# Kernel optimization log

Hardware: AMD Instinct MI355X
Metric: run time of the kernel (lower is better)

The kernel has to match this reference:

```python
import jax, jax.numpy as jnp
import numpy as np

D_MODEL, N, L_MAX, BATCH = 512, 64, 2048, 8


def _hippo_pq_lambda(n):
    # HiPPO-LegS matrix -> NPLR decomposition (numpy, done once at setup)
    i = np.arange(n)
    A = np.sqrt(2 * i + 1)[:, None] * np.sqrt(2 * i + 1)[None, :]
    A = np.tril(A, -1) + np.diag(i + 1.0)
    p0 = 0.5 * np.sqrt(2 * np.arange(1, n + 1) - 1.0)
    q0 = 2.0 * p0
    S = -A + p0[:, None] * q0[None, :]
    lam, V = np.linalg.eig(S)
    Vc = V.conj().T
    p = Vc @ p0.astype(np.complex128)
    q = Vc @ q0.astype(np.complex128)
    return lam, p, q


def _c2r(x):
    return np.stack([x.real, x.imag], axis=-1).astype(np.float32)


def setup_inputs() -> dict:
    key = jax.random.key(0)
    ks = jax.random.split(key, 6)
    lam, p, q = _hippo_pq_lambda(N)
    log_step_scale = float(np.log(0.1) - np.log(0.001))
    xavier_std = (2.0 / (D_MODEL + N)) ** 0.5
    return {
        "u": jax.random.normal(ks[0], (BATCH, L_MAX, D_MODEL), jnp.float32),
        "lam": jnp.asarray(_c2r(lam)),            # (N, 2) complex-as-real
        "p": jnp.asarray(_c2r(p)),                # (N, 2)
        "q": jnp.asarray(_c2r(q)),                # (N, 2)
        "B": jax.random.normal(ks[1], (D_MODEL, N, 2), jnp.float32) * xavier_std,
        "Ct": jax.random.normal(ks[2], (D_MODEL, N, 2), jnp.float32) * xavier_std,
        "D": jnp.ones((D_MODEL,), jnp.float32),
        "log_step": jax.random.uniform(ks[3], (D_MODEL,), jnp.float32) * log_step_scale + float(np.log(0.001)),
        "W": jax.random.normal(ks[4], (D_MODEL, D_MODEL), jnp.float32) / (D_MODEL ** 0.5),
        "b": jnp.zeros((D_MODEL,), jnp.float32),
        "gamma": jnp.ones((D_MODEL,), jnp.float32),
        "beta": jnp.zeros((D_MODEL,), jnp.float32),
    }


def _cplx(x):
    return x[..., 0] + 1j * x[..., 1]


def _s4_kernel(lam, p, q, B, Ct, step, l_max):
    # Generating function of the DPLR SSM kernel evaluated at roots of unity,
    # then inverse FFT -> length-l_max convolution kernel K, shape (d_model, l_max).
    omega = jnp.exp(2j * jnp.pi * jnp.arange(l_max) / l_max)  # (L,)
    a0, a1 = jnp.conj(Ct), jnp.conj(q)   # (d,n), (n,)
    b0, b1 = B, p                        # (d,n), (n,)
    v = jnp.stack([
        a0 * b0,
        a0 * b1[None, :],
        a1[None, :] * b0,
        jnp.broadcast_to((a1 * b1)[None, :], B.shape),
    ])  # (4, d, n)
    f = (2.0 / step)[:, None] * ((1.0 - omega) / (1.0 + omega))[None, :]  # (d, L)
    r = 1.0 / (f[:, :, None] - lam)      # (d, L, n)  -- dominant intermediate
    k = jnp.einsum('kdn,dln->kdl', v, r) # 4 Cauchy dots in one contraction
    at_roots = (2.0 / (1.0 + omega)) * (k[0] - k[1] * (1.0 / (1.0 + k[3])) * k[2])
    return jnp.fft.ifft(at_roots, n=l_max, axis=-1).real  # (d, L)


def _s4_block(u, lam, p, q, B, Ct, D, log_step, W, b, gamma, beta):
    L = u.shape[1]
    K = _s4_kernel(_cplx(lam), _cplx(p), _cplx(q), _cplx(B), _cplx(Ct), jnp.exp(log_step), L)
    # non-circular convolution via zero-padded FFT
    ud = jnp.fft.rfft(jnp.pad(u, ((0, 0), (0, L), (0, 0))), axis=1)   # (b, L+1, d)
    Kd = jnp.fft.rfft(jnp.pad(K, ((0, 0), (0, L))), axis=-1)          # (d, L+1)
    y = jnp.fft.irfft(ud * Kd.T[None], axis=1)[:, :L, :] + D * u      # S4Layer out
    y = jax.nn.gelu(y, approximate=False)                             # nn.GELU (exact)
    y = y @ W.T + b                                                   # nn.Linear
    y = y + u                                                         # Residual
    mu = jnp.mean(y, axis=-1, keepdims=True)                          # LayerNorm (post)
    var = jnp.mean((y - mu) ** 2, axis=-1, keepdims=True)
    return (y - mu) * jax.lax.rsqrt(var + 1e-5) * gamma + beta


def reference(u, lam, p, q, B, Ct, D, log_step, W, b, gamma, beta):
    return _s4_block(u, lam, p, q, B, Ct, D, log_step, W, b, gamma, beta)
```

## Files before the change

### kernel.cpp

```cpp
#include <hip/hip_runtime.h>
#include <math.h>

#define DM 512
#define NS 64
#define LS 2048
#define NB 8
#define LF 4096

typedef float2 cf;
using bf16x8 = __attribute__((ext_vector_type(8))) short;
using f32x4  = __attribute__((ext_vector_type(4))) float;

__device__ __forceinline__ cf cmul(cf a, cf b){ return make_float2(a.x*b.x - a.y*b.y, a.x*b.y + a.y*b.x); }
__device__ __forceinline__ cf cadd(cf a, cf b){ return make_float2(a.x+b.x, a.y+b.y); }
__device__ __forceinline__ cf csub(cf a, cf b){ return make_float2(a.x-b.x, a.y-b.y); }
__device__ __forceinline__ cf cconjf(cf a){ return make_float2(a.x, -a.y); }
__device__ __forceinline__ cf cscalef(cf a, float s){ return make_float2(a.x*s, a.y*s); }
__device__ __forceinline__ cf cdiv_fast(cf a, cf b){
  float inv = __builtin_amdgcn_rcpf(b.x*b.x + b.y*b.y);
  return make_float2((a.x*b.x + a.y*b.y)*inv, (a.y*b.x - a.x*b.y)*inv);
}

__device__ __forceinline__ float gelu_f(float x){
  return 0.5f*x*(1.0f + erff(x*0.7071067811865475f));
}

__device__ __forceinline__ ushort f2bf(float x){
  uint u = __float_as_uint(x);
  return (ushort)((u + 0x7fffu + ((u>>16)&1u)) >> 16);
}

__device__ __forceinline__ float2 f2add(float2 a, float2 b){ return make_float2(a.x+b.x, a.y+b.y); }
__device__ __forceinline__ float2 f2mul(float2 a, float2 b){ return make_float2(a.x*b.x, a.y*b.y); }
__device__ __forceinline__ float2 f2fma(float2 a, float2 b, float2 c){
  return make_float2(fmaf(a.x,b.x,c.x), fmaf(a.y,b.y,c.y));
}
__device__ __forceinline__ float2 splat2(float s){ return make_float2(s,s); }
__device__ __forceinline__ float2 rcp2(float2 a){
  return make_float2(__builtin_amdgcn_rcpf(a.x), __builtin_amdgcn_rcpf(a.y));
}

template<int N, int T, bool INV>
__device__ float2* fft_stockham4(float2* a, float2* b, int tid) {
  float2* src = a; float2* dst = b;
  const float base = (INV ? 6.283185307179586f : -6.283185307179586f) / (float)N;
  int m = 1;
  while (m * 4 <= N) {
    __syncthreads();
    #pragma unroll
    for (int ii = 0; ii < N/4/T; ii++) {
      int i = tid + ii*T;
      int j = i & ~(m-1);
      float2 c0 = src[i];
      float2 c1 = src[i + N/4];
      float2 c2 = src[i + 2*(N/4)];
      float2 c3 = src[i + 3*(N/4)];
      float2 s02 = cadd(c0,c2), d02 = csub(c0,c2);
      float2 s13 = cadd(c1,c3), d13 = csub(c1,c3);
      float2 jd13 = INV ? make_float2(-d13.y, d13.x) : make_float2(d13.y, -d13.x);
      float2 y0 = cadd(s02, s13);
      float2 y1 = cadd(d02, jd13);
      float2 y2 = csub(s02, s13);
      float2 y3 = csub(d02, jd13);
      float ang = base * (float)j;
      float sn, cs; __sincosf(ang, &sn, &cs);
      float2 w1 = make_float2(cs, sn);
      float2 w2 = cmul(w1, w1);
      float2 w3 = cmul(w2, w1);
      int o = i + 3*j;
      dst[o]       = y0;
      dst[o + m]   = cmul(y1, w1);
      dst[o + 2*m] = cmul(y2, w2);
      dst[o + 3*m] = cmul(y3, w3);
    }
    float2* t2 = src; src = dst; dst = t2;
    m <<= 2;
  }
  if (m < N) {
    __syncthreads();
    #pragma unroll
    for (int ii = 0; ii < N/2/T; ii++) {
      int i = tid + ii*T;
      int j = i & ~(m-1);
      float2 c0 = src[i], c1 = src[i + N/2];
      float ang = base * (float)j;
      float sn, cs; __sincosf(ang, &sn, &cs);
      float2 sum = cadd(c0,c1), dif = csub(c0,c1);
      dst[i + j]     = sum;
      dst[i + j + m] = cmul(dif, make_float2(cs,sn));
    }
    float2* t2 = src; src = dst; dst = t2;
    m <<= 1;
  }
  __syncthreads();
  return src;
}

__global__ __launch_bounds__(256) void transpose_kernel(
    const float* __restrict__ u, float* __restrict__ ut)
{
  __shared__ float tile[32][33];
  int b  = blockIdx.z;
  int t0 = blockIdx.x * 32;
  int d0 = blockIdx.y * 32;
  int tx = threadIdx.x & 31;
  int ty = threadIdx.x >> 5;
  #pragma unroll
  for (int r = 0; r < 32; r += 8)
    tile[ty + r][tx] = u[((size_t)b*LS + t0 + ty + r)*DM + d0 + tx];
  __syncthreads();
  #pragma unroll
  for (int r = 0; r < 32; r += 8)
    ut[((size_t)b*DM + d0 + ty + r)*LS + t0 + tx] = tile[tx][ty + r];
}

__global__ __launch_bounds__(256) void cauchy_kernel(
    const float* __restrict__ lam_g, const float* __restrict__ p_g,
    const float* __restrict__ q_g,   const float* __restrict__ B_g,
    const float* __restrict__ Ct_g,  const float* __restrict__ logstep_g,
    float2* __restrict__ at)
{
  __shared__ float tab[NS][12];
  int d     = blockIdx.x;
  int chunk = blockIdx.y;
  int tid = threadIdx.x;
  float tos = 2.0f / expf(logstep_g[d]);
  float invtos = __builtin_amdgcn_rcpf(tos);

  if (tid < NS) {
    int n = tid;
    float lx = lam_g[2*n], ly = lam_g[2*n+1];
    cf pn   = make_float2(p_g[2*n],   p_g[2*n+1]);
    cf qn   = make_float2(q_g[2*n],   q_g[2*n+1]);
    cf Bdn  = make_float2(B_g[(d*NS+n)*2],  B_g[(d*NS+n)*2+1]);
    cf Cdn  = make_float2(Ct_g[(d*NS+n)*2], Ct_g[(d*NS+n)*2+1]);
    cf a0 = cconjf(Cdn);
    cf a1 = cconjf(qn);
    cf w0 = cmul(a0, Bdn);
    cf w1 = cmul(a0, pn);
    cf w2 = cmul(a1, Bdn);
    cf w3 = cmul(a1, pn);
    tab[n][0] = -lx;  tab[n][1] = ly;   tab[n][2] = lx*lx; tab[n][3] = w0.x;
    tab[n][4] = w0.y; tab[n][5] = w1.x; tab[n][6] = w1.y;  tab[n][7] = w2.x;
    tab[n][8] = w2.y; tab[n][9] = w3.x; tab[n][10] = w3.y; tab[n][11] = 0.f;
  }

  float2 g2[2];
  #pragma unroll
  for (int sp = 0; sp < 2; sp++) {
    float gg[2];
    #pragma unroll
    for (int h = 0; h < 2; h++) {
      int l = chunk*1024 + (2*sp + h)*256 + tid;
      float half_ang = 3.14159265358979323846f * (float)l / (float)LS;
      float sn, cs;
      sincosf(half_ang, &sn, &cs);
      gg[h] = tos * (sn / cs);
    }
    g2[sp] = make_float2(gg[0], gg[1]);
  }
  __syncthreads();

  float2 k0x[2], k0y[2], k1x[2], k1y[2], k2x[2], k2y[2], k3x[2], k3y[2];
  #pragma unroll
  for (int sp = 0; sp < 2; sp++) {
    k0x[sp] = splat2(0.f); k0y[sp] = splat2(0.f);
    k1x[sp] = splat2(0.f); k1y[sp] = splat2(0.f);
    k2x[sp] = splat2(0.f); k2y[sp] = splat2(0.f);
    k3x[sp] = splat2(0.f); k3y[sp] = splat2(0.f);
  }

  #pragma unroll 2
  for (int n = 0; n < NS; n++) {
    float4 t0 = *reinterpret_cast<const float4*>(&tab[n][0]);
    float4 t1 = *reinterpret_cast<const float4*>(&tab[n][4]);
    float4 t2 = *reinterpret_cast<const float4*>(&tab[n][8]);
    #pragma unroll
    for (int sp = 0; sp < 2; sp++) {
      float2 e   = f2add(g2[sp], splat2(t0.y));
      float2 mag = f2fma(e, e, splat2(t0.z));
      float2 inv = rcp2(mag);
      float2 rx  = f2mul(splat2(t0.x), inv);
      float2 ry  = f2mul(e, inv);
      k0x[sp] = f2fma(splat2(t0.w), rx, k0x[sp]);
      k0x[sp] = f2fma(splat2(-t1.x), ry, k0x[sp]);
      k0y[sp] = f2fma(splat2(t0.w), ry, k0y[sp]);
      k0y[sp] = f2fma(splat2(t1.x), rx, k0y[sp]);
      k1x[sp] = f2fma(splat2(t1.y), rx, k1x[sp]);
      k1x[sp] = f2fma(splat2(-t1.z), ry, k1x[sp]);
      k1y[sp] = f2fma(splat2(t1.y), ry, k1y[sp]);
      k1y[sp] = f2fma(splat2(t1.z), rx, k1y[sp]);
      k2x[sp] = f2fma(splat2(t1.w), rx, k2x[sp]);
      k2x[sp] = f2fma(splat2(-t2.x), ry, k2x[sp]);
      k2y[sp] = f2fma(splat2(t1.w), ry, k2y[sp]);
      k2y[sp] = f2fma(splat2(t2.x), rx, k2y[sp]);
      k3x[sp] = f2fma(splat2(t2.y), rx, k3x[sp]);
      k3x[sp] = f2fma(splat2(-t2.z), ry, k3x[sp]);
      k3y[sp] = f2fma(splat2(t2.y), ry, k3y[sp]);
      k3y[sp] = f2fma(splat2(t2.z), rx, k3y[sp]);
    }
  }

  #pragma unroll
  for (int sp = 0; sp < 2; sp++) {
    #pragma unroll
    for (int h = 0; h < 2; h++) {
      int l = chunk*1024 + (2*sp + h)*256 + tid;
      float gv = (h == 0) ? g2[sp].x : g2[sp].y;
      cf k0 = make_float2(h==0?k0x[sp].x:k0x[sp].y, h==0?k0y[sp].x:k0y[sp].y);
      cf k1 = make_float2(h==0?k1x[sp].x:k1x[sp].y, h==0?k1y[sp].x:k1y[sp].y);
      cf k2 = make_float2(h==0?k2x[sp].x:k2x[sp].y, h==0?k2y[sp].x:k2y[sp].y);
      cf k3 = make_float2(h==0?k3x[sp].x:k3x[sp].y, h==0?k3y[sp].x:k3y[sp].y);
      cf t1c = cdiv_fast(cmul(k1, k2), make_float2(1.0f + k3.x, k3.y));
      cf inner = csub(k0, t1c);
      cf c2 = make_float2(1.0f, -gv * invtos);
      at[(size_t)d*LS + l] = cmul(c2, inner);
    }
  }
}

__global__ __launch_bounds__(512) void kfft_kernel(
    const float2* __restrict__ at, float2* __restrict__ Kf)
{
  __shared__ float2 bufA[LS];
  __shared__ float2 bufB[LS];
  int tid = threadIdx.x;
  int d0 = blockIdx.x * 2;
  const float2* at0 = at + (size_t)d0*LS;
  const float2* at1 = at0 + LS;
  float2* Kf0 = Kf + (size_t)d0*LF;
  float2* Kf1 = Kf0 + LF;

  #pragma unroll
  for (int s = 0; s < 4; s++) {
    int k = tid + s*512;
    int nk = (LS - k) & (LS - 1);
    cf a0k = at0[k], a0n = at0[nk];
    cf a1k = at1[k], a1n = at1[nk];
    cf H0 = make_float2(0.5f*(a0k.x + a0n.x), 0.5f*(a0k.y - a0n.y));
    cf H1 = make_float2(0.5f*(a1k.x + a1n.x), 0.5f*(a1k.y - a1n.y));
    Kf0[k] = H0;
    Kf1[k] = H1;
    bufA[k] = make_float2(H0.x - H1.y, H0.y + H1.x);
  }
  float2* res = fft_stockham4<LS, 512, true>(bufA, bufB, tid);
  float2* other = (res == bufA) ? bufB : bufA;
  #pragma unroll
  for (int s = 0; s < 4; s++) {
    int t = tid + s*512;
    float ang = 3.14159265358979323846f * (float)t / (float)LS;
    float sn, cs;
    __sincosf(ang, &sn, &cs);
    cf Kc = cscalef(res[t], 1.0f/(float)LS);
    other[t] = cmul(Kc, make_float2(cs, -sn));
  }
  float2* G = fft_stockham4<LS, 512, false>(other, res, tid);
  #pragma unroll
  for (int s = 0; s < 2; s++) {
    int k = tid + s*512;
    int rk = LS - 1 - k;
    cf Gk = G[k], Gr = G[rk];
    cf F0 = make_float2(0.5f*(Gk.x + Gr.x), 0.5f*(Gk.y - Gr.y));
    cf F1 = make_float2(0.5f*(Gk.y + Gr.y), 0.5f*(Gr.x - Gk.x));
    Kf0[LS + k]  = F0;
    Kf0[LS + rk] = cconjf(F0);
    Kf1[LS + k]  = F1;
    Kf1[LS + rk] = cconjf(F1);
  }
}

__global__ __launch_bounds__(512) void conv_kernel(
    const float* __restrict__ ut, const float2* __restrict__ Kf,
    const float* __restrict__ Dv, ushort* __restrict__ gb)
{
  __shared__ float2 bufA[LS];
  __shared__ float2 bufB[LS];
  int tid = threadIdx.x;
  int d0 = blockIdx.x * 2;
  int b  = blockIdx.y;
  const float* u0p = ut + ((size_t)b*DM + d0)*LS;
  const float* u1p = u0p + LS;
  const float2* Kf0 = Kf + (size_t)d0 * LF;
  const float2* Kf1 = Kf0 + LF;
  float u0r[4], u1r[4];
  #pragma unroll
  for (int s = 0; s < 4; s++) {
    int t = tid + s*512;
    u0r[s] = u0p[t]; u1r[s] = u1p[t];
    bufA[t] = make_float2(u0r[s], u1r[s]);
  }

  float2* Z  = fft_stockham4<LS, 512, false>(bufA, bufB, tid);
  float2* Wb = (Z == bufA) ? bufB : bufA;
  #pragma unroll
  for (int s = 0; s < 4; s++) {
    int mq = tid + s*512;
    int mm = (LS - mq) & (LS - 1);
    cf Za = Z[mq], Zb = Z[mm];
    cf U0 = make_float2(0.5f*(Za.x + Zb.x), 0.5f*(Za.y - Zb.y));
    cf U1 = make_float2(0.5f*(Za.y + Zb.y), 0.5f*(Zb.x - Za.x));
    cf Y0 = cmul(U0, Kf0[mq]);
    cf Y1 = cmul(U1, Kf1[mq]);
    Wb[mq] = make_float2(Y0.x - Y1.y, Y0.y + Y1.x);
  }
  float2* A = fft_stockham4<LS, 512, true>(Wb, Z, tid);
  float2 areg[4];
  #pragma unroll
  for (int s = 0; s < 4; s++) areg[s] = A[tid + s*512];

  float2* st = (A == bufA) ? bufB : bufA;
  #pragma unroll
  for (int s = 0; s < 4; s++) {
    int t = tid + s*512;
    float ang = -3.14159265358979323846f * (float)t / (float)LS;
    float sn, cs; __sincosf(ang, &sn, &cs);
    cf z = make_float2(u0r[s], u1r[s]);
    st[t] = cmul(z, make_float2(cs, sn));
  }
  float2* Z2  = fft_stockham4<LS, 512, false>(st, A, tid);
  float2* Wb2 = (Z2 == bufA) ? bufB : bufA;
  #pragma unroll
  for (int s = 0; s < 4; s++) {
    int mq = tid + s*512;
    int mm = LS - 1 - mq;
    cf Za = Z2[mq], Zb = Z2[mm];
    cf U0 = make_float2(0.5f*(Za.x + Zb.x), 0.5f*(Za.y - Zb.y));
    cf U1 = make_float2(0.5f*(Za.y + Zb.y), 0.5f*(Zb.x - Za.x));
    cf Y0 = cmul(U0, Kf0[LS + mq]);
    cf Y1 = cmul(U1, Kf1[LS + mq]);
    Wb2[mq] = make_float2(Y0.x - Y1.y, Y0.y + Y1.x);
  }
  float2* C = fft_stockham4<LS, 512, true>(Wb2, Z2, tid);

  float dv0 = Dv[d0], dv1 = Dv[d0+1];
  ushort* g0 = gb + ((size_t)b*DM + d0)*LS;
  ushort* g1 = g0 + LS;
  #pragma unroll
  for (int s = 0; s < 4; s++) {
    int t = tid + s*512;
    float ang = 3.14159265358979323846f * (float)t / (float)LS;
    float sn, cs; __sincosf(ang, &sn, &cs);
    cf c = C[t];
    cf bb = cmul(c, make_float2(cs, sn));
    float y0 = (areg[s].x + bb.x) * (1.0f/LF) + dv0 * u0r[s];
    float y1 = (areg[s].y + bb.y) * (1.0f/LF) + dv1 * u1r[s];
    g0[t] = f2bf(gelu_f(y0));
    g1[t] = f2bf(gelu_f(y1));
  }
}

__global__ __launch_bounds__(256) void transposeT_kernel(
    const ushort* __restrict__ gb, ushort* __restrict__ gt)
{
  __shared__ ushort tile[64][65];
  int b  = blockIdx.z;
  int t0 = blockIdx.x * 64;
  int d0 = blockIdx.y * 64;
  int tx = threadIdx.x & 31;
  int ty = threadIdx.x >> 5;
  #pragma unroll
  for (int r = 0; r < 8; r++) {
    int d = ty + r*8;
    uint v = *reinterpret_cast<const uint*>(&gb[((size_t)b*DM + d0 + d)*LS + t0 + tx*2]);
    tile[d][tx*2]   = (ushort)(v & 0xffffu);
    tile[d][tx*2+1] = (ushort)(v >> 16);
  }
  __syncthreads();
  #pragma unroll
  for (int r = 0; r < 8; r++) {
    int t = ty + r*8;
    uint lo = tile[tx*2][t];
    uint hi = tile[tx*2+1][t];
    *reinterpret_cast<uint*>(&gt[((size_t)b*LS + t0 + t)*DM + d0 + tx*2]) = lo | (hi << 16);
  }
}

__global__ __launch_bounds__(256) void wb_kernel(
    const float* __restrict__ W, ushort* __restrict__ Wb)
{
  int i = (blockIdx.x*256 + threadIdx.x)*4;
  float4 v = *reinterpret_cast<const float4*>(W + i);
  uint2 o;
  o.x = (uint)f2bf(v.x) | ((uint)f2bf(v.y) << 16);
  o.y = (uint)f2bf(v.z) | ((uint)f2bf(v.w) << 16);
  *reinterpret_cast<uint2*>(Wb + i) = o;
}

__global__ __launch_bounds__(256) void mfma_gemm_kernel(
    const ushort* __restrict__ gt, const ushort* __restrict__ Wbm,
    const float* __restrict__ bias, const float* __restrict__ u,
    float* __restrict__ out)
{
  __shared__ ushort As[128*64];
  __shared__ ushort Bs[128*64];
  int tid = threadIdx.x;
  int b  = blockIdx.z;
  int t0 = blockIdx.x * 128;
  int j0 = blockIdx.y * 128;
  int wid = tid >> 6, lane = tid & 63;
  int wm = wid >> 1, wn = wid & 1;
  int m = lane & 15, q = lane >> 4;

  f32x4 acc[4][4];
  #pragma unroll
  for (int i = 0; i < 4; i++)
    #pragma unroll
    for (int j = 0; j < 4; j++)
      acc[i][j] = (f32x4){0.f, 0.f, 0.f, 0.f};

  const ushort* Ag = gt + ((size_t)b*LS + t0)*DM;

  for (int k0 = 0; k0 < DM; k0 += 64) {
    #pragma unroll
    for (int i = 0; i < 4; i++) {
      int idx = tid + i*256;
      int r = idx >> 3, g = idx & 7;
      uint4 va = *reinterpret_cast<const uint4*>(Ag + (size_t)r*DM + k0 + g*8);
      *reinterpret_cast<uint4*>(&As[r*64 + ((g ^ (r&7))*8)]) = va;
      uint4 vb = *reinterpret_cast<const uint4*>(Wbm + (size_t)(j0 + r)*DM + k0 + g*8);
      *reinterpret_cast<uint4*>(&Bs[r*64 + ((g ^ (r&7))*8)]) = vb;
    }
    __syncthreads();
    #pragma unroll
    for (int kk = 0; kk < 64; kk += 32) {
      int gk = (kk >> 3) + q;
      bf16x8 af[4], bfr[4];
      #pragma unroll
      for (int mi = 0; mi < 4; mi++) {
        int row = wm*64 + mi*16 + m;
        af[mi] = *reinterpret_cast<const bf16x8*>(&As[row*64 + ((gk ^ (row&7))*8)]);
      }
      #pragma unroll
      for (int ni = 0; ni < 4; ni++) {
        int row = wn*64 + ni*16 + m;
        bfr[ni] = *reinterpret_cast<const bf16x8*>(&Bs[row*64 + ((gk ^ (row&7))*8)]);
      }
      #pragma unroll
      for (int mi = 0; mi < 4; mi++)
        #pragma unroll
        for (int ni = 0; ni < 4; ni++)
          acc[mi][ni] = __builtin_amdgcn_mfma_f32_16x16x32_bf16(af[mi], bfr[ni], acc[mi][ni], 0, 0, 0);
    }
    __syncthreads();
  }

  #pragma unroll
  for (int mi = 0; mi < 4; mi++) {
    #pragma unroll
    for (int ni = 0; ni < 4; ni++) {
      int col = j0 + wn*64 + ni*16 + m;
      float bb = bias[col];
      #pragma unroll
      for (int jj = 0; jj < 4; jj++) {
        int row = t0 + wm*64 + mi*16 + q*4 + jj;
        size_t off = ((size_t)b*LS + row)*DM + col;
        out[off] = acc[mi][ni][jj] + bb + u[off];
      }
    }
  }
}

__global__ __launch_bounds__(256) void ln_kernel(
    float* __restrict__ out, const float* __restrict__ gamma,
    const float* __restrict__ beta)
{
  int lane = threadIdx.x & 63;
  size_t row = (size_t)blockIdx.x * 4 + (threadIdx.x >> 6);
  float* p = out + row * DM;
  float4 v0 = *reinterpret_cast<float4*>(p + lane*8);
  float4 v1 = *reinterpret_cast<float4*>(p + lane*8 + 4);
  float sum = v0.x+v0.y+v0.z+v0.w + v1.x+v1.y+v1.z+v1.w;
  float sq  = v0.x*v0.x+v0.y*v0.y+v0.z*v0.z+v0.w*v0.w
            + v1.x*v1.x+v1.y*v1.y+v1.z*v1.z+v1.w*v1.w;
  #pragma unroll
  for (int off = 32; off >= 1; off >>= 1) {
    sum += __shfl_xor(sum, off, 64);
    sq  += __shfl_xor(sq,  off, 64);
  }
  float mu  = sum * (1.0f/DM);
  float var = sq  * (1.0f/DM) - mu*mu;
  float rs  = rsqrtf(var + 1e-5f);
  float4 g0 = *reinterpret_cast<const float4*>(gamma + lane*8);
  float4 g1 = *reinterpret_cast<const float4*>(gamma + lane*8 + 4);
  float4 b0 = *reinterpret_cast<const float4*>(beta + lane*8);
  float4 b1 = *reinterpret_cast<const float4*>(beta + lane*8 + 4);
  v0.x = (v0.x - mu)*rs*g0.x + b0.x;
  v0.y = (v0.y - mu)*rs*g0.y + b0.y;
  v0.z = (v0.z - mu)*rs*g0.z + b0.z;
  v0.w = (v0.w - mu)*rs*g0.w + b0.w;
  v1.x = (v1.x - mu)*rs*g1.x + b1.x;
  v1.y = (v1.y - mu)*rs*g1.y + b1.y;
  v1.z = (v1.z - mu)*rs*g1.z + b1.z;
  v1.w = (v1.w - mu)*rs*g1.w + b1.w;
  *reinterpret_cast<float4*>(p + lane*8)     = v0;
  *reinterpret_cast<float4*>(p + lane*8 + 4) = v1;
}

extern "C" void kernel_launch(void* const* d_in, const int* in_sizes, int n_in,
                              void* d_out, int out_size, void* d_ws, size_t ws_size,
                              hipStream_t stream) {
  const float* u       = (const float*)d_in[0];
  const float* lam     = (const float*)d_in[1];
  const float* p       = (const float*)d_in[2];
  const float* q       = (const float*)d_in[3];
  const float* B       = (const float*)d_in[4];
  const float* Ct      = (const float*)d_in[5];
  const float* Dv      = (const float*)d_in[6];
  const float* logstep = (const float*)d_in[7];
  const float* W       = (const float*)d_in[8];
  const float* bias    = (const float*)d_in[9];
  const float* gamma   = (const float*)d_in[10];
  const float* beta    = (const float*)d_in[11];
  float* out = (float*)d_out;

  char* wsb = (char*)d_ws;
  float2* Kf  = (float2*)wsb;
  ushort* gb  = (ushort*)(wsb + (size_t)16*1024*1024);
  ushort* Wbm = (ushort*)(wsb + (size_t)16*1024*1024);
  float2* at  = (float2*)(wsb + (size_t)32*1024*1024);
  ushort* gt  = (ushort*)(wsb + (size_t)32*1024*1024);
  float* ut = (float*)d_out;

  transpose_kernel<<<dim3(LS/32, DM/32, NB), 256, 0, stream>>>(u, ut);
  cauchy_kernel<<<dim3(DM, 2), 256, 0, stream>>>(lam, p, q, B, Ct, logstep, at);
  kfft_kernel<<<dim3(DM/2), 512, 0, stream>>>(at, Kf);
  conv_kernel<<<dim3(DM/2, NB), 512, 0, stream>>>(ut, Kf, Dv, gb);
  transposeT_kernel<<<dim3(LS/64, DM/64, NB), 256, 0, stream>>>(gb, gt);
  wb_kernel<<<dim3(DM*DM/1024), 256, 0, stream>>>(W, Wbm);
  mfma_gemm_kernel<<<dim3(LS/128, DM/128, NB), 256, 0, stream>>>(gt, Wbm, bias, u, out);
  ln_kernel<<<dim3(NB*LS/4), 256, 0, stream>>>(out, gamma, beta);
}
```

Baseline: 160.9 us.

## Switch shared-memory FFT to radix-8 Stockham with padded LDS and 256 threads

Replaces the radix-4 Stockham FFT with a radix-8 version plus radix-4/radix-2 tail stages. This roughly halves the number of LDS passes and barriers per 2048-point transform. Shared buffers get one float2 of padding every 32 elements to reduce LDS bank conflicts on strided accesses. The FFT kernels now run with 256 threads, each handling 8 elements, and conv_kernel gets an occupancy hint of 4. The trade-off is more registers per thread, which could lower occupancy.

```diff
diff --git a/kernel.cpp b/kernel.cpp
--- a/kernel.cpp
+++ b/kernel.cpp
@@ -6,6 +6,7 @@
 #define LS 2048
 #define NB 8
 #define LF 4096
+#define LSP (LS + (LS>>5))
 
 typedef float2 cf;
 using bf16x8 = __attribute__((ext_vector_type(8))) short;
@@ -30,6 +31,8 @@
   return (ushort)((u + 0x7fffu + ((u>>16)&1u)) >> 16);
 }
 
+__device__ __forceinline__ int lp(int x){ return x + (x >> 5); }
+
 __device__ __forceinline__ float2 f2add(float2 a, float2 b){ return make_float2(a.x+b.x, a.y+b.y); }
 __device__ __forceinline__ float2 f2mul(float2 a, float2 b){ return make_float2(a.x*b.x, a.y*b.y); }
 __device__ __forceinline__ float2 f2fma(float2 a, float2 b, float2 c){
@@ -41,23 +44,67 @@
 }
 
 template<int N, int T, bool INV>
-__device__ float2* fft_stockham4(float2* a, float2* b, int tid) {
+__device__ float2* fft_stockham8(float2* a, float2* b, int tid) {
   float2* src = a; float2* dst = b;
   const float base = (INV ? 6.283185307179586f : -6.283185307179586f) / (float)N;
+  const float sg = INV ? 1.0f : -1.0f;
+  const float C8 = 0.70710678118654752f;
   int m = 1;
-  while (m * 4 <= N) {
+  while (m * 8 <= N) {
+    __syncthreads();
+    #pragma unroll
+    for (int ii = 0; ii < N/8/T; ii++) {
+      int i = tid + ii*T;
+      int j = i & ~(m-1);
+      float2 c[8];
+      #pragma unroll
+      for (int t = 0; t < 8; t++) c[t] = src[lp(i + t*(N/8))];
+      float2 s0=cadd(c[0],c[4]), d0=csub(c[0],c[4]);
+      float2 s1=cadd(c[1],c[5]), d1=csub(c[1],c[5]);
+      float2 s2=cadd(c[2],c[6]), d2=csub(c[2],c[6]);
+      float2 s3=cadd(c[3],c[7]), d3=csub(c[3],c[7]);
+      float2 t1 = make_float2(C8*(d1.x - sg*d1.y), C8*(d1.y + sg*d1.x));
+      float2 t2 = make_float2(-sg*d2.y, sg*d2.x);
+      float2 t3 = make_float2(-C8*(d3.x + sg*d3.y), C8*(sg*d3.x - d3.y));
+      float2 es=cadd(s0,s2), ed=csub(s0,s2), fs=cadd(s1,s3), fd=csub(s1,s3);
+      float2 je = make_float2(-sg*fd.y, sg*fd.x);
+      float2 y0=cadd(es,fs), y4=csub(es,fs);
+      float2 y2=cadd(ed,je), y6=csub(ed,je);
+      float2 os=cadd(d0,t2), od=csub(d0,t2), ps=cadd(t1,t3), pd=csub(t1,t3);
+      float2 jo = make_float2(-sg*pd.y, sg*pd.x);
+      float2 y1=cadd(os,ps), y5=csub(os,ps);
+      float2 y3=cadd(od,jo), y7=csub(od,jo);
+      float ang = base*(float)j;
+      float sn, cs; __sincosf(ang, &sn, &cs);
+      float2 w1 = make_float2(cs, sn);
+      float2 w2 = cmul(w1,w1), w3 = cmul(w2,w1), w4 = cmul(w2,w2);
+      float2 w5 = cmul(w4,w1), w6 = cmul(w4,w2), w7 = cmul(w4,w3);
+      int o = i + 7*j;
+      dst[lp(o)]       = y0;
+      dst[lp(o + m)]   = cmul(y1,w1);
+      dst[lp(o + 2*m)] = cmul(y2,w2);
+      dst[lp(o + 3*m)] = cmul(y3,w3);
+      dst[lp(o + 4*m)] = cmul(y4,w4);
+      dst[lp(o + 5*m)] = cmul(y5,w5);
+      dst[lp(o + 6*m)] = cmul(y6,w6);
+      dst[lp(o + 7*m)] = cmul(y7,w7);
+    }
+    float2* tswap = src; src = dst; dst = tswap;
+    m <<= 3;
+  }
+  if (m * 4 <= N) {
     __syncthreads();
     #pragma unroll
     for (int ii = 0; ii < N/4/T; ii++) {
       int i = tid + ii*T;
       int j = i & ~(m-1);
-      float2 c0 = src[i];
-      float2 c1 = src[i + N/4];
-      float2 c2 = src[i + 2*(N/4)];
-      float2 c3 = src[i + 3*(N/4)];
+      float2 c0 = src[lp(i)];
+      float2 c1 = src[lp(i + N/4)];
+      float2 c2 = src[lp(i + 2*(N/4))];
+      float2 c3 = src[lp(i + 3*(N/4))];
       float2 s02 = cadd(c0,c2), d02 = csub(c0,c2);
       float2 s13 = cadd(c1,c3), d13 = csub(c1,c3);
-      float2 jd13 = INV ? make_float2(-d13.y, d13.x) : make_float2(d13.y, -d13.x);
+      float2 jd13 = make_float2(-sg*d13.y, sg*d13.x);
       float2 y0 = cadd(s02, s13);
       float2 y1 = cadd(d02, jd13);
       float2 y2 = csub(s02, s13);
@@ -68,28 +115,28 @@
       float2 w2 = cmul(w1, w1);
       float2 w3 = cmul(w2, w1);
       int o = i + 3*j;
-      dst[o]       = y0;
-      dst[o + m]   = cmul(y1, w1);
-      dst[o + 2*m] = cmul(y2, w2);
-      dst[o + 3*m] = cmul(y3, w3);
-    }
-    float2* t2 = src; src = dst; dst = t2;
+      dst[lp(o)]       = y0;
+      dst[lp(o + m)]   = cmul(y1, w1);
+      dst[lp(o + 2*m)] = cmul(y2, w2);
+      dst[lp(o + 3*m)] = cmul(y3, w3);
+    }
+    float2* tswap = src; src = dst; dst = tswap;
     m <<= 2;
   }
-  if (m < N) {
+  if (m * 2 <= N) {
     __syncthreads();
     #pragma unroll
     for (int ii = 0; ii < N/2/T; ii++) {
       int i = tid + ii*T;
       int j = i & ~(m-1);
-      float2 c0 = src[i], c1 = src[i + N/2];
+      float2 c0 = src[lp(i)], c1 = src[lp(i + N/2)];
       float ang = base * (float)j;
       float sn, cs; __sincosf(ang, &sn, &cs);
       float2 sum = cadd(c0,c1), dif = csub(c0,c1);
-      dst[i + j]     = sum;
-      dst[i + j + m] = cmul(dif, make_float2(cs,sn));
-    }
-    float2* t2 = src; src = dst; dst = t2;
+      dst[lp(i + j)]     = sum;
+      dst[lp(i + j + m)] = cmul(dif, make_float2(cs,sn));
+    }
+    float2* tswap = src; src = dst; dst = tswap;
     m <<= 1;
   }
   __syncthreads();
@@ -219,11 +266,11 @@
   }
 }
 
-__global__ __launch_bounds__(512) void kfft_kernel(
+__global__ __launch_bounds__(256) void kfft_kernel(
     const float2* __restrict__ at, float2* __restrict__ Kf)
 {
-  __shared__ float2 bufA[LS];
-  __shared__ float2 bufB[LS];
+  __shared__ float2 bufA[LSP];
+  __shared__ float2 bufB[LSP];
   int tid = threadIdx.x;
   int d0 = blockIdx.x * 2;
   const float2* at0 = at + (size_t)d0*LS;
@@ -232,8 +279,8 @@
   float2* Kf1 = Kf0 + LF;
 
   #pragma unroll
-  for (int s = 0; s < 4; s++) {
-    int k = tid + s*512;
+  for (int s = 0; s < 8; s++) {
+    int k = tid + s*256;
     int nk = (LS - k) & (LS - 1);
     cf a0k = at0[k], a0n = at0[nk];
     cf a1k = at1[k], a1n = at1[nk];
@@ -241,25 +288,25 @@
     cf H1 = make_float2(0.5f*(a1k.x + a1n.x), 0.5f*(a1k.y - a1n.y));
     Kf0[k] = H0;
     Kf1[k] = H1;
-    bufA[k] = make_float2(H0.x - H1.y, H0.y + H1.x);
-  }
-  float2* res = fft_stockham4<LS, 512, true>(bufA, bufB, tid);
+    bufA[lp(k)] = make_float2(H0.x - H1.y, H0.y + H1.x);
+  }
+  float2* res = fft_stockham8<LS, 256, true>(bufA, bufB, tid);
   float2* other = (res == bufA) ? bufB : bufA;
   #pragma unroll
-  for (int s = 0; s < 4; s++) {
-    int t = tid + s*512;
+  for (int s = 0; s < 8; s++) {
+    int t = tid + s*256;
     float ang = 3.14159265358979323846f * (float)t / (float)LS;
     float sn, cs;
     __sincosf(ang, &sn, &cs);
-    cf Kc = cscalef(res[t], 1.0f/(float)LS);
-    other[t] = cmul(Kc, make_float2(cs, -sn));
-  }
-  float2* G = fft_stockham4<LS, 512, false>(other, res, tid);
-  #pragma unroll
-  for (int s = 0; s < 2; s++) {
-    int k = tid + s*512;
+    cf Kc = cscalef(res[lp(t)], 1.0f/(float)LS);
+    other[lp(t)] = cmul(Kc, make_float2(cs, -sn));
+  }
+  float2* G = fft_stockham8<LS, 256, false>(other, res, tid);
+  #pragma unroll
+  for (int s = 0; s < 4; s++) {
+    int k = tid + s*256;
     int rk = LS - 1 - k;
-    cf Gk = G[k], Gr = G[rk];
+    cf Gk = G[lp(k)], Gr = G[lp(rk)];
     cf F0 = make_float2(0.5f*(Gk.x + Gr.x), 0.5f*(Gk.y - Gr.y));
     cf F1 = make_float2(0.5f*(Gk.y + Gr.y), 0.5f*(Gr.x - Gk.x));
     Kf0[LS + k]  = F0;
@@ -269,12 +316,12 @@
   }
 }
 
-__global__ __launch_bounds__(512) void conv_kernel(
+__global__ __launch_bounds__(256, 4) void conv_kernel(
     const float* __restrict__ ut, const float2* __restrict__ Kf,
     const float* __restrict__ Dv, ushort* __restrict__ gb)
 {
-  __shared__ float2 bufA[LS];
-  __shared__ float2 bufB[LS];
+  __shared__ float2 bufA[LSP];
+  __shared__ float2 bufB[LSP];
   int tid = threadIdx.x;
   int d0 = blockIdx.x * 2;
   int b  = blockIdx.y;
@@ -282,65 +329,65 @@
   const float* u1p = u0p + LS;
   const float2* Kf0 = Kf + (size_t)d0 * LF;
   const float2* Kf1 = Kf0 + LF;
-  float u0r[4], u1r[4];
-  #pragma unroll
-  for (int s = 0; s < 4; s++) {
-    int t = tid + s*512;
+  float u0r[8], u1r[8];
+  #pragma unroll
+  for (int s = 0; s < 8; s++) {
+    int t = tid + s*256;
     u0r[s] = u0p[t]; u1r[s] = u1p[t];
-    bufA[t] = make_float2(u0r[s], u1r[s]);
-  }
-
-  float2* Z  = fft_stockham4<LS, 512, false>(bufA, bufB, tid);
+    bufA[lp(t)] = make_float2(u0r[s], u1r[s]);
+  }
+
+  float2* Z  = fft_stockham8<LS, 256, false>(bufA, bufB, tid);
   float2* Wb = (Z == bufA) ? bufB : bufA;
   #pragma unroll
-  for (int s = 0; s < 4; s++) {
-    int mq = tid + s*512;
+  for (int s = 0; s < 8; s++) {
+    int mq = tid + s*256;
     int mm = (LS - mq) & (LS - 1);
-    cf Za = Z[mq], Zb = Z[mm];
+    cf Za = Z[lp(mq)], Zb = Z[lp(mm)];
     cf U0 = make_float2(0.5f*(Za.x + Zb.x), 0.5f*(Za.y - Zb.y));
     cf U1 = make_float2(0.5f*(Za.y + Zb.y), 0.5f*(Zb.x - Za.x));
     cf Y0 = cmul(U0, Kf0[mq]);
     cf Y1 = cmul(U1, Kf1[mq]);
-    Wb[mq] = make_float2(Y0.x - Y1.y, Y0.y + Y1.x);
-  }
-  float2* A = fft_stockham4<LS, 512, true>(Wb, Z, tid);
-  float2 areg[4];
-  #pragma unroll
-  for (int s = 0; s < 4; s++) areg[s] = A[tid + s*512];
+    Wb[lp(mq)] = make_float2(Y0.x - Y1.y, Y0.y + Y1.x);
+  }
+  float2* A = fft_stockham8<LS, 256, true>(Wb, Z, tid);
+  float2 areg[8];
+  #pragma unroll
+  for (int s = 0; s < 8; s++) areg[s] = A[lp(tid + s*256)];
 
   float2* st = (A == bufA) ? bufB : bufA;
   #pragma unroll
-  for (int s = 0; s < 4; s++) {
-    int t = tid + s*512;
+  for (int s = 0; s < 8; s++) {
+    int t = tid + s*256;
     float ang = -3.14159265358979323846f * (float)t / (float)LS;
     float sn, cs; __sincosf(ang, &sn, &cs);
     cf z = make_float2(u0r[s], u1r[s]);
-    st[t] = cmul(z, make_float2(cs, sn));
-  }
-  float2* Z2  = fft_stockham4<LS, 512, false>(st, A, tid);
+    st[lp(t)] = cmul(z, make_float2(cs, sn));
+  }
+  float2* Z2  = fft_stockham8<LS, 256, false>(st, A, tid);
   float2* Wb2 = (Z2 == bufA) ? bufB : bufA;
   #pragma unroll
-  for (int s = 0; s < 4; s++) {
-    int mq = tid + s*512;
+  for (int s = 0; s < 8; s++) {
+    int mq = tid + s*256;
     int mm = LS - 1 - mq;
-    cf Za = Z2[mq], Zb = Z2[mm];
+    cf Za = Z2[lp(mq)], Zb = Z2[lp(mm)];
     cf U0 = make_float2(0.5f*(Za.x + Zb.x), 0.5f*(Za.y - Zb.y));
     cf U1 = make_float2(0.5f*(Za.y + Zb.y), 0.5f*(Zb.x - Za.x));
     cf Y0 = cmul(U0, Kf0[LS + mq]);
     cf Y1 = cmul(U1, Kf1[LS + mq]);
-    Wb2[mq] = make_float2(Y0.x - Y1.y, Y0.y + Y1.x);
-  }
-  float2* C = fft_stockham4<LS, 512, true>(Wb2, Z2, tid);
+    Wb2[lp(mq)] = make_float2(Y0.x - Y1.y, Y0.y + Y1.x);
+  }
+  float2* C = fft_stockham8<LS, 256, true>(Wb2, Z2, tid);
 
   float dv0 = Dv[d0], dv1 = Dv[d0+1];
   ushort* g0 = gb + ((size_t)b*DM + d0)*LS;
   ushort* g1 = g0 + LS;
   #pragma unroll
-  for (int s = 0; s < 4; s++) {
-    int t = tid + s*512;
+  for (int s = 0; s < 8; s++) {
+    int t = tid + s*256;
     float ang = 3.14159265358979323846f * (float)t / (float)LS;
     float sn, cs; __sincosf(ang, &sn, &cs);
-    cf c = C[t];
+    cf c = C[lp(t)];
     cf bb = cmul(c, make_float2(cs, sn));
     float y0 = (areg[s].x + bb.x) * (1.0f/LF) + dv0 * u0r[s];
     float y1 = (areg[s].y + bb.y) * (1.0f/LF) + dv1 * u1r[s];
@@ -523,8 +570,8 @@
 
   transpose_kernel<<<dim3(LS/32, DM/32, NB), 256, 0, stream>>>(u, ut);
   cauchy_kernel<<<dim3(DM, 2), 256, 0, stream>>>(lam, p, q, B, Ct, logstep, at);
-  kfft_kernel<<<dim3(DM/2), 512, 0, stream>>>(at, Kf);
-  conv_kernel<<<dim3(DM/2, NB), 512, 0, stream>>>(ut, Kf, Dv, gb);
+  kfft_kernel<<<dim3(DM/2), 256, 0, stream>>>(at, Kf);
+  conv_kernel<<<dim3(DM/2, NB), 256, 0, stream>>>(ut, Kf, Dv, gb);
   transposeT_kernel<<<dim3(LS/64, DM/64, NB), 256, 0, stream>>>(gb, gt);
   wb_kernel<<<dim3(DM*DM/1024), 256, 0, stream>>>(W, Wbm);
   mfma_gemm_kernel<<<dim3(LS/128, DM/128, NB), 256, 0, stream>>>(gt, Wbm, bias, u, out);
```

New measurement: 171.3 us. 6.5% more time.
